# Kernel optimization log

Hardware: AMD Instinct MI355X
Metric: run time of the kernel (lower is better)

Reference implementation:

```python
import jax, jax.numpy as jnp
import numpy as np

N, T, C = 8, 2048, 1024   # batch, seq_len, n_embd (== num_cls)
NUM_CLS = 1024
LID, TL = 6, 12


def setup_inputs() -> dict:
    key = jax.random.key(0)
    ks = jax.random.split(key, 5)
    s = 1.0 / np.sqrt(C)
    x = jax.random.normal(ks[0], (N, T, C), jnp.float32)
    Wk = jax.random.normal(ks[1], (C, C), jnp.float32) * s
    Wv = jax.random.normal(ks[2], (C, C), jnp.float32) * s
    Wr = jax.random.normal(ks[3], (C, C), jnp.float32) * s
    Wo = jax.random.normal(ks[4], (NUM_CLS, C), jnp.float32) * s
    # faithful time-parameter initialization from __init__
    r0 = LID / (TL - 1)            # ratio_0_to_1
    r1 = 1.0 - LID / TL            # ratio_1_to_almost0
    ddd = (np.arange(C, dtype=np.float32) / C).reshape(1, 1, C)
    time_mix_k = jnp.asarray(ddd ** r1)
    time_mix_v = jnp.asarray(ddd ** r1 + 0.3 * r0)
    time_mix_r = jnp.asarray(ddd ** (0.5 * r1))
    time_decay = jnp.zeros((C,), jnp.float32)                 # decay_speed init
    time_first = jnp.full((C,), np.log(0.3), jnp.float32)
    last_x = jnp.zeros((N, 1, C), jnp.float32)                # init_x repeated
    state = jnp.zeros((N, 3, 1, C), jnp.float32)              # init_state repeated
    return {"x": x, "it": 0, "Wk": Wk, "Wv": Wv, "Wr": Wr, "Wo": Wo,
            "time_mix_k": time_mix_k, "time_mix_v": time_mix_v,
            "time_mix_r": time_mix_r, "time_decay": time_decay,
            "time_first": time_first, "last_x": last_x, "state": state}


def _wkv_with_eps(w, u, k, v, state):
    """Numerically-stabilized RWKV wkv scan. k,v: (N,T,C); state: (N,3,1,C)."""
    alpha = state[:, 0, -1]  # (N,C)
    beta = state[:, 1, -1]
    eps = state[:, 2, -1]

    def step(carry, kv):
        a, b, e = carry
        kt, vt = kv                      # each (N,C)
        ukt = u + kt
        tau = jnp.maximum(ukt, e)
        e1 = jnp.exp(e - tau)
        e2 = jnp.exp(ukt - tau)
        wkv_t = (e1 * a + e2 * vt) / (e1 * b + e2)
        w_eps = e - w
        e_n = jnp.maximum(w_eps, kt)
        e1n = jnp.exp(w_eps - e_n)
        e2n = jnp.exp(kt - e_n)
        return (e1n * a + e2n * vt, e1n * b + e2n, e_n), wkv_t

    kT = jnp.swapaxes(k, 0, 1)  # (T,N,C)
    vT = jnp.swapaxes(v, 0, 1)
    (alpha, beta, eps), wkv = jax.lax.scan(step, (alpha, beta, eps), (kT, vT))
    wkv = jnp.swapaxes(wkv, 0, 1)  # (N,T,C)
    last_state = jnp.stack([alpha, beta, eps], axis=1)[:, :, None, :]  # (N,3,1,C)
    return wkv, last_state


def reference(x, it, Wk, Wv, Wr, Wo, time_mix_k, time_mix_v, time_mix_r,
              time_decay, time_first, last_x, state):
    # time-mix blend (last_x = init_x zeros, broadcast over T as in the source)
    k = (x * time_mix_k + last_x * (1.0 - time_mix_k)) @ Wk.T
    v = (x * time_mix_v + last_x * (1.0 - time_mix_v)) @ Wv.T
    r = (x * time_mix_r + last_x * (1.0 - time_mix_r)) @ Wr.T
    sr = jax.nn.sigmoid(r)
    w = jnp.exp(time_decay)
    u = time_first
    wkv, _last_state = _wkv_with_eps(w, u, k, v, state)
    rwkv = (wkv * sr) @ Wo.T  # (N,T,NUM_CLS)
    return rwkv
```

## Files before the change

### kernel.cpp

```cpp
#include <hip/hip_runtime.h>
#include <hip/hip_bf16.h>
#include <stdint.h>


typedef float f4 __attribute__((ext_vector_type(4)));
typedef short bh8 __attribute__((ext_vector_type(8)));
typedef unsigned int u32;
typedef unsigned short u16;

__device__ __forceinline__ u32 cvt2bf(float a, float b) {
    __hip_bfloat162 h = __float22bfloat162_rn(make_float2(a, b));
    u32 u; __builtin_memcpy(&u, &h, 4); return u;
}
__device__ __forceinline__ float b2f(u16 u) {
    u32 x = (u32)u << 16; float f; __builtin_memcpy(&f, &x, 4); return f;
}
__device__ __forceinline__ u16 f2b(float f) {
    __hip_bfloat16 h = __float2bfloat16(f);
    u16 u; __builtin_memcpy(&u, &h, 2); return u;
}
__device__ __forceinline__ void gld_lds16(const void* g, void* l) {
    __builtin_amdgcn_global_load_lds(
        (const __attribute__((address_space(1))) u32*)g,
        (__attribute__((address_space(3))) u32*)l, 16, 0, 0);
}

template <int EPI>
__global__ __launch_bounds__(256, 2) void gemm_bt(
    const u16* __restrict__ A, const u16* __restrict__ B, void* __restrict__ Yv)
{
    __shared__ __align__(16) u16 As[128 * 32];
    __shared__ __align__(16) u16 Bs[128 * 32];

    const int tid  = threadIdx.x;
    const int w    = tid >> 6;
    const int lane = tid & 63;
    const int m0 = blockIdx.x * 128;
    const int n0 = blockIdx.y * 128;

    const int srow = w * 32 + (lane >> 2);
    const int slot = lane & 3;
    const int chk  = slot ^ ((srow >> 1) & 3);
    const u16* gA0 = A + (size_t)(m0 + srow) * 1024 + chk * 8;
    const u16* gA1 = gA0 + (size_t)16 * 1024;
    const u16* gB0 = B + (size_t)(n0 + srow) * 1024 + chk * 8;
    const u16* gB1 = gB0 + (size_t)16 * 1024;
    u16* lA0 = As + (w * 32) * 32;
    u16* lA1 = lA0 + 16 * 32;
    u16* lB0 = Bs + (w * 32) * 32;
    u16* lB1 = lB0 + 16 * 32;

    const int fr   = lane & 15;
    const int quad = lane >> 4;
    const int wm = (w & 1) * 64;
    const int wn = (w >> 1) * 64;
    const int sp = quad ^ ((fr >> 1) & 3);
    const int aoff = (wm + fr) * 32 + sp * 8;
    const int boff = (wn + fr) * 32 + sp * 8;

    f4 acc[4][4];
#pragma unroll
    for (int i = 0; i < 4; i++)
#pragma unroll
        for (int j = 0; j < 4; j++) { f4 z = {0.f, 0.f, 0.f, 0.f}; acc[i][j] = z; }

    for (int kk = 0; kk < 1024; kk += 32) {
        gld_lds16(gA0 + kk, lA0);
        gld_lds16(gA1 + kk, lA1);
        gld_lds16(gB0 + kk, lB0);
        gld_lds16(gB1 + kk, lB1);
        __syncthreads();
        bh8 af[4], bf[4];
#pragma unroll
        for (int i = 0; i < 4; i++) af[i] = *(const bh8*)(As + aoff + i * 16 * 32);
#pragma unroll
        for (int j = 0; j < 4; j++) bf[j] = *(const bh8*)(Bs + boff + j * 16 * 32);
#pragma unroll
        for (int i = 0; i < 4; i++)
#pragma unroll
            for (int j = 0; j < 4; j++)
                acc[i][j] = __builtin_amdgcn_mfma_f32_16x16x32_bf16(af[i], bf[j], acc[i][j], 0, 0, 0);
        __syncthreads();
    }

    const int rb = quad * 4;
#pragma unroll
    for (int i = 0; i < 4; i++)
#pragma unroll
        for (int j = 0; j < 4; j++)
#pragma unroll
            for (int r = 0; r < 4; r++) {
                float v = acc[i][j][r];
                size_t row = (size_t)(m0 + wm + i * 16 + rb + r);
                size_t col = (size_t)(n0 + wn + j * 16 + fr);
                if (EPI == 0) {
                    ((float*)Yv)[row * 1024 + col] = v;
                } else if (EPI == 1) {
                    ((u16*)Yv)[row * 1024 + col] = f2b(v);
                } else {
                    ((u16*)Yv)[row * 1024 + col] = f2b(__fdividef(1.0f, 1.0f + __expf(-v)));
                }
            }
}

__global__ __launch_bounds__(256) void prep3(
    const float* __restrict__ x, const float* __restrict__ lastx,
    const float* __restrict__ tmk, const float* __restrict__ tmv, const float* __restrict__ tmr,
    u16* __restrict__ Xk, u16* __restrict__ Xv, u16* __restrict__ Xr)
{
    int idx = blockIdx.x * 256 + threadIdx.x;
    int e = idx << 2;
    int c = e & 1023;
    int n = e >> 21;
    f4 xv = *(const f4*)(x + e);
    f4 lx = *(const f4*)(lastx + (n << 10) + c);
    f4 mk = *(const f4*)(tmk + c);
    f4 mv = *(const f4*)(tmv + c);
    f4 mr = *(const f4*)(tmr + c);
    f4 k = lx + (xv - lx) * mk;
    f4 v = lx + (xv - lx) * mv;
    f4 r = lx + (xv - lx) * mr;
    *(uint2*)(Xk + e) = make_uint2(cvt2bf(k.x, k.y), cvt2bf(k.z, k.w));
    *(uint2*)(Xv + e) = make_uint2(cvt2bf(v.x, v.y), cvt2bf(v.z, v.w));
    *(uint2*)(Xr + e) = make_uint2(cvt2bf(r.x, r.y), cvt2bf(r.z, r.w));
}

__global__ __launch_bounds__(256) void prep1(
    const float* __restrict__ x, const float* __restrict__ lastx,
    const float* __restrict__ tm, u16* __restrict__ X)
{
    int idx = blockIdx.x * 256 + threadIdx.x;
    int e = idx << 2;
    int c = e & 1023;
    int n = e >> 21;
    f4 xv = *(const f4*)(x + e);
    f4 lx = *(const f4*)(lastx + (n << 10) + c);
    f4 m  = *(const f4*)(tm + c);
    f4 k = lx + (xv - lx) * m;
    *(uint2*)(X + e) = make_uint2(cvt2bf(k.x, k.y), cvt2bf(k.z, k.w));
}

__global__ __launch_bounds__(256) void convw(const float* __restrict__ s, u16* __restrict__ d) {
    int idx = blockIdx.x * 256 + threadIdx.x;
    int e = idx << 2;
    f4 v = *(const f4*)(s + e);
    *(uint2*)(d + e) = make_uint2(cvt2bf(v.x, v.y), cvt2bf(v.z, v.w));
}

__global__ __launch_bounds__(256) void wkv_pass1(
    const u16* __restrict__ Kp, const u16* __restrict__ Vp,
    const float* __restrict__ tdec,
    float* __restrict__ Ca, float* __restrict__ Cb, float* __restrict__ Ce)
{
    int tid = blockIdx.x * 256 + threadIdx.x;
    int c = tid & 1023;
    int chunk = (tid >> 10) & 31;
    int n = tid >> 15;
    float w = __expf(tdec[c]);
    int base = (n * 2048 + chunk * 64) * 1024 + c;
    float ca = 0.f, cb = 0.f, ce = -1e30f;
#pragma unroll 8
    for (int i = 0; i < 64; i++) {
        float kt = b2f(Kp[base + (i << 10)]);
        float vt = b2f(Vp[base + (i << 10)]);
        float ed = ce - w;
        float en = fmaxf(ed, kt);
        float f1 = __expf(ed - en);
        float f2 = __expf(kt - en);
        ca = fmaf(f1, ca, f2 * vt);
        cb = fmaf(f1, cb, f2);
        ce = en;
    }
    int oidx = ((n * 32 + chunk) << 10) + c;
    Ca[oidx] = ca; Cb[oidx] = cb; Ce[oidx] = ce;
}

__global__ __launch_bounds__(256) void wkv_pass2(
    const float* __restrict__ state, const float* __restrict__ tdec,
    const float* __restrict__ Ca, const float* __restrict__ Cb, const float* __restrict__ Ce,
    float* __restrict__ Sa, float* __restrict__ Sb, float* __restrict__ Se)
{
    int tid = blockIdx.x * 256 + threadIdx.x;
    int c = tid & 1023;
    int n = tid >> 10;
    float a = state[(n * 3 + 0) * 1024 + c];
    float b = state[(n * 3 + 1) * 1024 + c];
    float e = state[(n * 3 + 2) * 1024 + c];
    float wL = __expf(tdec[c]) * 64.0f;
    for (int ch = 0; ch < 32; ++ch) {
        int idx = ((n * 32 + ch) << 10) + c;
        Sa[idx] = a; Sb[idx] = b; Se[idx] = e;
        float ce = Ce[idx];
        float ed = e - wL;
        float en = fmaxf(ed, ce);
        float f1 = __expf(ed - en);
        float f2 = __expf(ce - en);
        a = fmaf(f1, a, f2 * Ca[idx]);
        b = fmaf(f1, b, f2 * Cb[idx]);
        e = en;
    }
}

__global__ __launch_bounds__(256) void wkv_pass3(
    const u16* __restrict__ Kp, const u16* __restrict__ Vp, const u16* __restrict__ SRp,
    const float* __restrict__ Sa, const float* __restrict__ Sb, const float* __restrict__ Se,
    const float* __restrict__ tfirst, const float* __restrict__ tdec,
    u16* __restrict__ Pp)
{
    int tid = blockIdx.x * 256 + threadIdx.x;
    int c = tid & 1023;
    int chunk = (tid >> 10) & 31;
    int n = tid >> 15;
    int sidx = ((n * 32 + chunk) << 10) + c;
    float a = Sa[sidx], b = Sb[sidx], e = Se[sidx];
    float u = tfirst[c];
    float w = __expf(tdec[c]);
    int base = (n * 2048 + chunk * 64) * 1024 + c;
#pragma unroll 4
    for (int i = 0; i < 64; i++) {
        float kt = b2f(Kp[base + (i << 10)]);
        float vt = b2f(Vp[base + (i << 10)]);
        float st = b2f(SRp[base + (i << 10)]);
        float ukt = u + kt;
        float tau = fmaxf(ukt, e);
        float e1 = __expf(e - tau);
        float e2 = __expf(ukt - tau);
        float wkv = __fdividef(fmaf(e1, a, e2 * vt), fmaf(e1, b, e2));
        Pp[base + (i << 10)] = f2b(wkv * st);
        float ed = e - w;
        float en = fmaxf(ed, kt);
        float f1 = __expf(ed - en);
        float f2 = __expf(kt - en);
        a = fmaf(f1, a, f2 * vt);
        b = fmaf(f1, b, f2);
        e = en;
    }
}

extern "C" void kernel_launch(void* const* d_in, const int* in_sizes, int n_in,
                              void* d_out, int out_size, void* d_ws, size_t ws_size,
                              hipStream_t stream) {
    const float* x      = (const float*)d_in[0];
    const float* Wk     = (const float*)d_in[2];
    const float* Wv     = (const float*)d_in[3];
    const float* Wr     = (const float*)d_in[4];
    const float* Wo     = (const float*)d_in[5];
    const float* tmk    = (const float*)d_in[6];
    const float* tmv    = (const float*)d_in[7];
    const float* tmr    = (const float*)d_in[8];
    const float* tdec   = (const float*)d_in[9];
    const float* tfirst = (const float*)d_in[10];
    const float* lastx  = (const float*)d_in[11];
    const float* state  = (const float*)d_in[12];
    float* out = (float*)d_out;

    const size_t MB = 1024ull * 1024ull;
    char* ws = (char*)d_ws;
    u16* Kb  = (u16*)(ws);
    u16* Vb  = (u16*)(ws + 32 * MB);
    u16* SRb = (u16*)(ws + 64 * MB);

    dim3 g(128, 8), blk(256);
    const bool big = ws_size >= 206 * MB;

    if (big) {
        u16* Xk  = (u16*)(ws + 96 * MB);
        u16* Xv  = (u16*)(ws + 128 * MB);
        u16* Xr  = (u16*)(ws + 160 * MB);
        u16* Wkb = (u16*)(ws + 192 * MB);
        u16* Wvb = (u16*)(ws + 194 * MB);
        u16* Wrb = (u16*)(ws + 196 * MB);
        u16* Wob = (u16*)(ws + 198 * MB);
        float* Ca = (float*)(ws + 200 * MB);
        float* Cb = Ca + 262144;
        float* Ce = Cb + 262144;
        float* Sa = Ce + 262144;
        float* Sb = Sa + 262144;
        float* Se = Sb + 262144;
        u16* Pb = Xk;

        prep3<<<16384, blk, 0, stream>>>(x, lastx, tmk, tmv, tmr, Xk, Xv, Xr);
        convw<<<1024, blk, 0, stream>>>(Wk, Wkb);
        convw<<<1024, blk, 0, stream>>>(Wv, Wvb);
        convw<<<1024, blk, 0, stream>>>(Wr, Wrb);
        convw<<<1024, blk, 0, stream>>>(Wo, Wob);
        gemm_bt<1><<<g, blk, 0, stream>>>(Xk, Wkb, Kb);
        gemm_bt<1><<<g, blk, 0, stream>>>(Xv, Wvb, Vb);
        gemm_bt<2><<<g, blk, 0, stream>>>(Xr, Wrb, SRb);
        wkv_pass1<<<1024, blk, 0, stream>>>(Kb, Vb, tdec, Ca, Cb, Ce);
        wkv_pass2<<<32, blk, 0, stream>>>(state, tdec, Ca, Cb, Ce, Sa, Sb, Se);
        wkv_pass3<<<1024, blk, 0, stream>>>(Kb, Vb, SRb, Sa, Sb, Se, tfirst, tdec, Pb);
        gemm_bt<0><<<g, blk, 0, stream>>>(Pb, Wob, out);
    } else {
        u16* X   = (u16*)(ws + 96 * MB);
        u16* Wkb = (u16*)(ws + 128 * MB);
        u16* Wvb = (u16*)(ws + 130 * MB);
        u16* Wrb = (u16*)(ws + 132 * MB);
        u16* Wob = (u16*)(ws + 134 * MB);
        float* Ca = (float*)(ws + 136 * MB);
        float* Cb = Ca + 262144;
        float* Ce = Cb + 262144;
        float* Sa = Ce + 262144;
        float* Sb = Sa + 262144;
        float* Se = Sb + 262144;
        u16* Pb = X;

        convw<<<1024, blk, 0, stream>>>(Wk, Wkb);
        convw<<<1024, blk, 0, stream>>>(Wv, Wvb);
        convw<<<1024, blk, 0, stream>>>(Wr, Wrb);
        convw<<<1024, blk, 0, stream>>>(Wo, Wob);
        prep1<<<16384, blk, 0, stream>>>(x, lastx, tmk, X);
        gemm_bt<1><<<g, blk, 0, stream>>>(X, Wkb, Kb);
        prep1<<<16384, blk, 0, stream>>>(x, lastx, tmv, X);
        gemm_bt<1><<<g, blk, 0, stream>>>(X, Wvb, Vb);
        prep1<<<16384, blk, 0, stream>>>(x, lastx, tmr, X);
        gemm_bt<2><<<g, blk, 0, stream>>>(X, Wrb, SRb);
        wkv_pass1<<<1024, blk, 0, stream>>>(Kb, Vb, tdec, Ca, Cb, Ce);
        wkv_pass2<<<32, blk, 0, stream>>>(state, tdec, Ca, Cb, Ce, Sa, Sb, Se);
        wkv_pass3<<<1024, blk, 0, stream>>>(Kb, Vb, SRb, Sa, Sb, Se, tfirst, tdec, Pb);
        gemm_bt<0><<<g, blk, 0, stream>>>(Pb, Wob, out);
    }
}
```

Baseline: 392.5 us.

## Fold time-mix into weights, fuse K/V/R GEMMs, vectorize WKV scans

The time-mix blend is moved algebraically into the weights: x is converted to bf16 once, each Wk/Wv/Wr column is scaled by its mix vector, and the last_x term becomes a per-batch bias computed by a small reduction kernel. The three projection GEMMs become one launch over a 24-wide grid that reads a single bf16 x buffer and applies bias and sigmoid in the epilogue. The WKV pass1 and pass3 kernels now have each thread process two channels with 32-bit packed loads and stores, halving the grid. This removes three x-blend passes and their bf16 writes, at the cost of rounding the scaled weights to bf16 and adding an extra bias kernel.

Result: faster. 377.3 us (-3.9%).

```diff
diff --git a/kernel.cpp b/kernel.cpp
--- a/kernel.cpp
+++ b/kernel.cpp
@@ -25,18 +25,13 @@
         (__attribute__((address_space(3))) u32*)l, 16, 0, 0);
 }
 
-template <int EPI>
-__global__ __launch_bounds__(256, 2) void gemm_bt(
-    const u16* __restrict__ A, const u16* __restrict__ B, void* __restrict__ Yv)
-{
-    __shared__ __align__(16) u16 As[128 * 32];
-    __shared__ __align__(16) u16 Bs[128 * 32];
-
+__device__ __forceinline__ void gemm_core(
+    const u16* __restrict__ A, const u16* __restrict__ B,
+    int m0, int n0, u16* As, u16* Bs, f4 (&acc)[4][4])
+{
     const int tid  = threadIdx.x;
     const int w    = tid >> 6;
     const int lane = tid & 63;
-    const int m0 = blockIdx.x * 128;
-    const int n0 = blockIdx.y * 128;
 
     const int srow = w * 32 + (lane >> 2);
     const int slot = lane & 3;
@@ -58,12 +53,6 @@
     const int aoff = (wm + fr) * 32 + sp * 8;
     const int boff = (wn + fr) * 32 + sp * 8;
 
-    f4 acc[4][4];
-#pragma unroll
-    for (int i = 0; i < 4; i++)
-#pragma unroll
-        for (int j = 0; j < 4; j++) { f4 z = {0.f, 0.f, 0.f, 0.f}; acc[i][j] = z; }
-
     for (int kk = 0; kk < 1024; kk += 32) {
         gld_lds16(gA0 + kk, lA0);
         gld_lds16(gA1 + kk, lA1);
@@ -82,97 +71,166 @@
                 acc[i][j] = __builtin_amdgcn_mfma_f32_16x16x32_bf16(af[i], bf[j], acc[i][j], 0, 0, 0);
         __syncthreads();
     }
-
+}
+
+__global__ __launch_bounds__(256, 2) void gemm_kvr(
+    const u16* __restrict__ A, const u16* __restrict__ Wall, const float* __restrict__ bias,
+    u16* __restrict__ Kb, u16* __restrict__ Vb, u16* __restrict__ SRb)
+{
+    __shared__ __align__(16) u16 As[128 * 32];
+    __shared__ __align__(16) u16 Bs[128 * 32];
+    const int m0 = blockIdx.x * 128;
+    const int proj = blockIdx.y >> 3;
+    const int n0 = (blockIdx.y & 7) * 128;
+    const u16* B = Wall + (size_t)proj * 1048576;
+
+    f4 acc[4][4];
+#pragma unroll
+    for (int i = 0; i < 4; i++)
+#pragma unroll
+        for (int j = 0; j < 4; j++) { f4 z = {0.f, 0.f, 0.f, 0.f}; acc[i][j] = z; }
+    gemm_core(A, B, m0, n0, As, Bs, acc);
+
+    u16* Y = proj == 0 ? Kb : (proj == 1 ? Vb : SRb);
+    const int lane = threadIdx.x & 63;
+    const int w = threadIdx.x >> 6;
+    const int fr = lane & 15, quad = lane >> 4;
+    const int wm = (w & 1) * 64, wn = (w >> 1) * 64;
     const int rb = quad * 4;
+    const int batch = m0 >> 11;
+    float bv[4];
+#pragma unroll
+    for (int j = 0; j < 4; j++) bv[j] = bias[proj * 8192 + batch * 1024 + n0 + wn + j * 16 + fr];
 #pragma unroll
     for (int i = 0; i < 4; i++)
 #pragma unroll
         for (int j = 0; j < 4; j++)
 #pragma unroll
             for (int r = 0; r < 4; r++) {
-                float v = acc[i][j][r];
+                float v = acc[i][j][r] + bv[j];
+                if (proj == 2) v = __fdividef(1.0f, 1.0f + __expf(-v));
                 size_t row = (size_t)(m0 + wm + i * 16 + rb + r);
                 size_t col = (size_t)(n0 + wn + j * 16 + fr);
-                if (EPI == 0) {
-                    ((float*)Yv)[row * 1024 + col] = v;
-                } else if (EPI == 1) {
-                    ((u16*)Yv)[row * 1024 + col] = f2b(v);
-                } else {
-                    ((u16*)Yv)[row * 1024 + col] = f2b(__fdividef(1.0f, 1.0f + __expf(-v)));
-                }
+                Y[row * 1024 + col] = f2b(v);
             }
 }
 
-__global__ __launch_bounds__(256) void prep3(
-    const float* __restrict__ x, const float* __restrict__ lastx,
-    const float* __restrict__ tmk, const float* __restrict__ tmv, const float* __restrict__ tmr,
-    u16* __restrict__ Xk, u16* __restrict__ Xv, u16* __restrict__ Xr)
-{
-    int idx = blockIdx.x * 256 + threadIdx.x;
-    int e = idx << 2;
-    int c = e & 1023;
-    int n = e >> 21;
-    f4 xv = *(const f4*)(x + e);
-    f4 lx = *(const f4*)(lastx + (n << 10) + c);
-    f4 mk = *(const f4*)(tmk + c);
-    f4 mv = *(const f4*)(tmv + c);
-    f4 mr = *(const f4*)(tmr + c);
-    f4 k = lx + (xv - lx) * mk;
-    f4 v = lx + (xv - lx) * mv;
-    f4 r = lx + (xv - lx) * mr;
-    *(uint2*)(Xk + e) = make_uint2(cvt2bf(k.x, k.y), cvt2bf(k.z, k.w));
-    *(uint2*)(Xv + e) = make_uint2(cvt2bf(v.x, v.y), cvt2bf(v.z, v.w));
-    *(uint2*)(Xr + e) = make_uint2(cvt2bf(r.x, r.y), cvt2bf(r.z, r.w));
-}
-
-__global__ __launch_bounds__(256) void prep1(
-    const float* __restrict__ x, const float* __restrict__ lastx,
-    const float* __restrict__ tm, u16* __restrict__ X)
-{
-    int idx = blockIdx.x * 256 + threadIdx.x;
-    int e = idx << 2;
-    int c = e & 1023;
-    int n = e >> 21;
-    f4 xv = *(const f4*)(x + e);
-    f4 lx = *(const f4*)(lastx + (n << 10) + c);
-    f4 m  = *(const f4*)(tm + c);
-    f4 k = lx + (xv - lx) * m;
-    *(uint2*)(X + e) = make_uint2(cvt2bf(k.x, k.y), cvt2bf(k.z, k.w));
-}
-
-__global__ __launch_bounds__(256) void convw(const float* __restrict__ s, u16* __restrict__ d) {
+__global__ __launch_bounds__(256, 2) void gemm_out(
+    const u16* __restrict__ A, const u16* __restrict__ B, float* __restrict__ Y)
+{
+    __shared__ __align__(16) u16 As[128 * 32];
+    __shared__ __align__(16) u16 Bs[128 * 32];
+    const int m0 = blockIdx.x * 128;
+    const int n0 = blockIdx.y * 128;
+    f4 acc[4][4];
+#pragma unroll
+    for (int i = 0; i < 4; i++)
+#pragma unroll
+        for (int j = 0; j < 4; j++) { f4 z = {0.f, 0.f, 0.f, 0.f}; acc[i][j] = z; }
+    gemm_core(A, B, m0, n0, As, Bs, acc);
+
+    const int lane = threadIdx.x & 63;
+    const int w = threadIdx.x >> 6;
+    const int fr = lane & 15, quad = lane >> 4;
+    const int wm = (w & 1) * 64, wn = (w >> 1) * 64;
+    const int rb = quad * 4;
+#pragma unroll
+    for (int i = 0; i < 4; i++)
+#pragma unroll
+        for (int j = 0; j < 4; j++)
+#pragma unroll
+            for (int r = 0; r < 4; r++) {
+                size_t row = (size_t)(m0 + wm + i * 16 + rb + r);
+                size_t col = (size_t)(n0 + wn + j * 16 + fr);
+                Y[row * 1024 + col] = acc[i][j][r];
+            }
+}
+
+__global__ __launch_bounds__(256) void convx(const float* __restrict__ s, u16* __restrict__ d) {
     int idx = blockIdx.x * 256 + threadIdx.x;
     int e = idx << 2;
     f4 v = *(const f4*)(s + e);
     *(uint2*)(d + e) = make_uint2(cvt2bf(v.x, v.y), cvt2bf(v.z, v.w));
 }
 
+__global__ __launch_bounds__(256) void prepw(
+    const float* __restrict__ Wk, const float* __restrict__ Wv,
+    const float* __restrict__ Wr, const float* __restrict__ Wo,
+    const float* __restrict__ tmk, const float* __restrict__ tmv, const float* __restrict__ tmr,
+    u16* __restrict__ Wall)
+{
+    int idx = blockIdx.x * 256 + threadIdx.x;
+    int e = idx << 2;
+    int wid = e >> 20;
+    int off = e & 1048575;
+    int c = e & 1023;
+    const float* src = wid == 0 ? Wk : (wid == 1 ? Wv : (wid == 2 ? Wr : Wo));
+    f4 v = *(const f4*)(src + off);
+    if (wid < 3) {
+        const float* m = wid == 0 ? tmk : (wid == 1 ? tmv : tmr);
+        v = v * *(const f4*)(m + c);
+    }
+    *(uint2*)(Wall + e) = make_uint2(cvt2bf(v.x, v.y), cvt2bf(v.z, v.w));
+}
+
+__global__ __launch_bounds__(256) void bias3(
+    const float* __restrict__ Wk, const float* __restrict__ Wv, const float* __restrict__ Wr,
+    const float* __restrict__ tmk, const float* __restrict__ tmv, const float* __restrict__ tmr,
+    const float* __restrict__ lastx, float* __restrict__ bias)
+{
+    int wid = blockIdx.x * 4 + (threadIdx.x >> 6);
+    int lane = threadIdx.x & 63;
+    int proj = wid >> 10;
+    int n = wid & 1023;
+    const float* W = proj == 0 ? Wk : (proj == 1 ? Wv : Wr);
+    const float* m = proj == 0 ? tmk : (proj == 1 ? tmv : tmr);
+    float acc[8];
+#pragma unroll
+    for (int b = 0; b < 8; b++) acc[b] = 0.f;
+    for (int c = lane; c < 1024; c += 64) {
+        float wc = W[n * 1024 + c] * (1.0f - m[c]);
+#pragma unroll
+        for (int b = 0; b < 8; b++) acc[b] = fmaf(lastx[b * 1024 + c], wc, acc[b]);
+    }
+#pragma unroll
+    for (int b = 0; b < 8; b++) {
+        float v = acc[b];
+#pragma unroll
+        for (int sh = 32; sh >= 1; sh >>= 1) v += __shfl_xor(v, sh);
+        if (lane == 0) bias[proj * 8192 + b * 1024 + n] = v;
+    }
+}
+
 __global__ __launch_bounds__(256) void wkv_pass1(
     const u16* __restrict__ Kp, const u16* __restrict__ Vp,
     const float* __restrict__ tdec,
     float* __restrict__ Ca, float* __restrict__ Cb, float* __restrict__ Ce)
 {
     int tid = blockIdx.x * 256 + threadIdx.x;
-    int c = tid & 1023;
-    int chunk = (tid >> 10) & 31;
-    int n = tid >> 15;
-    float w = __expf(tdec[c]);
+    int c = (tid & 511) << 1;
+    int chunk = (tid >> 9) & 31;
+    int n = tid >> 14;
+    float w0 = __expf(tdec[c]), w1 = __expf(tdec[c + 1]);
     int base = (n * 2048 + chunk * 64) * 1024 + c;
-    float ca = 0.f, cb = 0.f, ce = -1e30f;
-#pragma unroll 8
+    float a0 = 0.f, b0 = 0.f, e0 = -1e30f;
+    float a1 = 0.f, b1 = 0.f, e1 = -1e30f;
+#pragma unroll 4
     for (int i = 0; i < 64; i++) {
-        float kt = b2f(Kp[base + (i << 10)]);
-        float vt = b2f(Vp[base + (i << 10)]);
-        float ed = ce - w;
-        float en = fmaxf(ed, kt);
-        float f1 = __expf(ed - en);
-        float f2 = __expf(kt - en);
-        ca = fmaf(f1, ca, f2 * vt);
-        cb = fmaf(f1, cb, f2);
-        ce = en;
+        u32 ku = *(const u32*)(Kp + base + (i << 10));
+        u32 vu = *(const u32*)(Vp + base + (i << 10));
+        float k0 = b2f((u16)ku), k1 = b2f((u16)(ku >> 16));
+        float v0 = b2f((u16)vu), v1 = b2f((u16)(vu >> 16));
+        float en0 = fmaxf(e0 - w0, k0);
+        float f10 = __expf(e0 - w0 - en0), f20 = __expf(k0 - en0);
+        a0 = fmaf(f10, a0, f20 * v0); b0 = fmaf(f10, b0, f20); e0 = en0;
+        float en1 = fmaxf(e1 - w1, k1);
+        float f11 = __expf(e1 - w1 - en1), f21 = __expf(k1 - en1);
+        a1 = fmaf(f11, a1, f21 * v1); b1 = fmaf(f11, b1, f21); e1 = en1;
     }
     int oidx = ((n * 32 + chunk) << 10) + c;
-    Ca[oidx] = ca; Cb[oidx] = cb; Ce[oidx] = ce;
+    *(float2*)(Ca + oidx) = make_float2(a0, a1);
+    *(float2*)(Cb + oidx) = make_float2(b0, b1);
+    *(float2*)(Ce + oidx) = make_float2(e0, e1);
 }
 
 __global__ __launch_bounds__(256) void wkv_pass2(
@@ -191,9 +249,8 @@
         int idx = ((n * 32 + ch) << 10) + c;
         Sa[idx] = a; Sb[idx] = b; Se[idx] = e;
         float ce = Ce[idx];
-        float ed = e - wL;
-        float en = fmaxf(ed, ce);
-        float f1 = __expf(ed - en);
+        float en = fmaxf(e - wL, ce);
+        float f1 = __expf(e - wL - en);
         float f2 = __expf(ce - en);
         a = fmaf(f1, a, f2 * Ca[idx]);
         b = fmaf(f1, b, f2 * Cb[idx]);
@@ -208,32 +265,36 @@
     u16* __restrict__ Pp)
 {
     int tid = blockIdx.x * 256 + threadIdx.x;
-    int c = tid & 1023;
-    int chunk = (tid >> 10) & 31;
-    int n = tid >> 15;
+    int c = (tid & 511) << 1;
+    int chunk = (tid >> 9) & 31;
+    int n = tid >> 14;
     int sidx = ((n * 32 + chunk) << 10) + c;
-    float a = Sa[sidx], b = Sb[sidx], e = Se[sidx];
-    float u = tfirst[c];
-    float w = __expf(tdec[c]);
+    float a0 = Sa[sidx], b0 = Sb[sidx], e0 = Se[sidx];
+    float a1 = Sa[sidx + 1], b1 = Sb[sidx + 1], e1 = Se[sidx + 1];
+    float u0 = tfirst[c], u1 = tfirst[c + 1];
+    float w0 = __expf(tdec[c]), w1 = __expf(tdec[c + 1]);
     int base = (n * 2048 + chunk * 64) * 1024 + c;
-#pragma unroll 4
+#pragma unroll 2
     for (int i = 0; i < 64; i++) {
-        float kt = b2f(Kp[base + (i << 10)]);
-        float vt = b2f(Vp[base + (i << 10)]);
-        float st = b2f(SRp[base + (i << 10)]);
-        float ukt = u + kt;
-        float tau = fmaxf(ukt, e);
-        float e1 = __expf(e - tau);
-        float e2 = __expf(ukt - tau);
-        float wkv = __fdividef(fmaf(e1, a, e2 * vt), fmaf(e1, b, e2));
-        Pp[base + (i << 10)] = f2b(wkv * st);
-        float ed = e - w;
-        float en = fmaxf(ed, kt);
-        float f1 = __expf(ed - en);
-        float f2 = __expf(kt - en);
-        a = fmaf(f1, a, f2 * vt);
-        b = fmaf(f1, b, f2);
-        e = en;
+        u32 ku = *(const u32*)(Kp + base + (i << 10));
+        u32 vu = *(const u32*)(Vp + base + (i << 10));
+        u32 su = *(const u32*)(SRp + base + (i << 10));
+        float k0 = b2f((u16)ku), k1 = b2f((u16)(ku >> 16));
+        float v0 = b2f((u16)vu), v1 = b2f((u16)(vu >> 16));
+        float s0 = b2f((u16)su), s1 = b2f((u16)(su >> 16));
+        float t0 = fmaxf(u0 + k0, e0);
+        float x10 = __expf(e0 - t0), x20 = __expf(u0 + k0 - t0);
+        float wkv0 = __fdividef(fmaf(x10, a0, x20 * v0), fmaf(x10, b0, x20));
+        float t1 = fmaxf(u1 + k1, e1);
+        float x11 = __expf(e1 - t1), x21 = __expf(u1 + k1 - t1);
+        float wkv1 = __fdividef(fmaf(x11, a1, x21 * v1), fmaf(x11, b1, x21));
+        *(u32*)(Pp + base + (i << 10)) = (u32)f2b(wkv0 * s0) | ((u32)f2b(wkv1 * s1) << 16);
+        float en0 = fmaxf(e0 - w0, k0);
+        float f10 = __expf(e0 - w0 - en0), f20 = __expf(k0 - en0);
+        a0 = fmaf(f10, a0, f20 * v0); b0 = fmaf(f10, b0, f20); e0 = en0;
+        float en1 = fmaxf(e1 - w1, k1);
+        float f11 = __expf(e1 - w1 - en1), f21 = __expf(k1 - en1);
+        a1 = fmaf(f11, a1, f21 * v1); b1 = fmaf(f11, b1, f21); e1 = en1;
     }
 }
 
@@ -256,68 +317,27 @@
 
     const size_t MB = 1024ull * 1024ull;
     char* ws = (char*)d_ws;
-    u16* Kb  = (u16*)(ws);
-    u16* Vb  = (u16*)(ws + 32 * MB);
-    u16* SRb = (u16*)(ws + 64 * MB);
-
-    dim3 g(128, 8), blk(256);
-    const bool big = ws_size >= 206 * MB;
-
-    if (big) {
-        u16* Xk  = (u16*)(ws + 96 * MB);
-        u16* Xv  = (u16*)(ws + 128 * MB);
-        u16* Xr  = (u16*)(ws + 160 * MB);
-        u16* Wkb = (u16*)(ws + 192 * MB);
-        u16* Wvb = (u16*)(ws + 194 * MB);
-        u16* Wrb = (u16*)(ws + 196 * MB);
-        u16* Wob = (u16*)(ws + 198 * MB);
-        float* Ca = (float*)(ws + 200 * MB);
-        float* Cb = Ca + 262144;
-        float* Ce = Cb + 262144;
-        float* Sa = Ce + 262144;
-        float* Sb = Sa + 262144;
-        float* Se = Sb + 262144;
-        u16* Pb = Xk;
-
-        prep3<<<16384, blk, 0, stream>>>(x, lastx, tmk, tmv, tmr, Xk, Xv, Xr);
-        convw<<<1024, blk, 0, stream>>>(Wk, Wkb);
-        convw<<<1024, blk, 0, stream>>>(Wv, Wvb);
-        convw<<<1024, blk, 0, stream>>>(Wr, Wrb);
-        convw<<<1024, blk, 0, stream>>>(Wo, Wob);
-        gemm_bt<1><<<g, blk, 0, stream>>>(Xk, Wkb, Kb);
-        gemm_bt<1><<<g, blk, 0, stream>>>(Xv, Wvb, Vb);
-        gemm_bt<2><<<g, blk, 0, stream>>>(Xr, Wrb, SRb);
-        wkv_pass1<<<1024, blk, 0, stream>>>(Kb, Vb, tdec, Ca, Cb, Ce);
-        wkv_pass2<<<32, blk, 0, stream>>>(state, tdec, Ca, Cb, Ce, Sa, Sb, Se);
-        wkv_pass3<<<1024, blk, 0, stream>>>(Kb, Vb, SRb, Sa, Sb, Se, tfirst, tdec, Pb);
-        gemm_bt<0><<<g, blk, 0, stream>>>(Pb, Wob, out);
-    } else {
-        u16* X   = (u16*)(ws + 96 * MB);
-        u16* Wkb = (u16*)(ws + 128 * MB);
-        u16* Wvb = (u16*)(ws + 130 * MB);
-        u16* Wrb = (u16*)(ws + 132 * MB);
-        u16* Wob = (u16*)(ws + 134 * MB);
-        float* Ca = (float*)(ws + 136 * MB);
-        float* Cb = Ca + 262144;
-        float* Ce = Cb + 262144;
-        float* Sa = Ce + 262144;
-        float* Sb = Sa + 262144;
-        float* Se = Sb + 262144;
-        u16* Pb = X;
-
-        convw<<<1024, blk, 0, stream>>>(Wk, Wkb);
-        convw<<<1024, blk, 0, stream>>>(Wv, Wvb);
-        convw<<<1024, blk, 0, stream>>>(Wr, Wrb);
-        convw<<<1024, blk, 0, stream>>>(Wo, Wob);
-        prep1<<<16384, blk, 0, stream>>>(x, lastx, tmk, X);
-        gemm_bt<1><<<g, blk, 0, stream>>>(X, Wkb, Kb);
-        prep1<<<16384, blk, 0, stream>>>(x, lastx, tmv, X);
-        gemm_bt<1><<<g, blk, 0, stream>>>(X, Wvb, Vb);
-        prep1<<<16384, blk, 0, stream>>>(x, lastx, tmr, X);
-        gemm_bt<2><<<g, blk, 0, stream>>>(X, Wrb, SRb);
-        wkv_pass1<<<1024, blk, 0, stream>>>(Kb, Vb, tdec, Ca, Cb, Ce);
-        wkv_pass2<<<32, blk, 0, stream>>>(state, tdec, Ca, Cb, Ce, Sa, Sb, Se);
-        wkv_pass3<<<1024, blk, 0, stream>>>(Kb, Vb, SRb, Sa, Sb, Se, tfirst, tdec, Pb);
-        gemm_bt<0><<<g, blk, 0, stream>>>(Pb, Wob, out);
-    }
-}
+    u16* Kb   = (u16*)(ws);
+    u16* Vb   = (u16*)(ws + 32 * MB);
+    u16* SRb  = (u16*)(ws + 64 * MB);
+    u16* xb   = (u16*)(ws + 96 * MB);
+    u16* Wall = (u16*)(ws + 128 * MB);
+    float* bias = (float*)(ws + 136 * MB);
+    float* Ca = (float*)(ws + 137 * MB);
+    float* Cb = Ca + 262144;
+    float* Ce = Cb + 262144;
+    float* Sa = Ce + 262144;
+    float* Sb = Sa + 262144;
+    float* Se = Sb + 262144;
+    u16* Pb = xb;
+
+    dim3 blk(256);
+    convx<<<16384, blk, 0, stream>>>(x, xb);
+    prepw<<<4096, blk, 0, stream>>>(Wk, Wv, Wr, Wo, tmk, tmv, tmr, Wall);
+    bias3<<<768, blk, 0, stream>>>(Wk, Wv, Wr, tmk, tmv, tmr, lastx, bias);
+    gemm_kvr<<<dim3(128, 24), blk, 0, stream>>>(xb, Wall, bias, Kb, Vb, SRb);
+    wkv_pass1<<<512, blk, 0, stream>>>(Kb, Vb, tdec, Ca, Cb, Ce);
+    wkv_pass2<<<32, blk, 0, stream>>>(state, tdec, Ca, Cb, Ce, Sa, Sb, Se);
+    wkv_pass3<<<512, blk, 0, stream>>>(Kb, Vb, SRb, Sa, Sb, Se, tfirst, tdec, Pb);
+    gemm_out<<<dim3(128, 8), blk, 0, stream>>>(Pb, Wall + 3145728, out);
+}
```
